# Kernel optimization log

Hardware: AMD Instinct MI355X
Metric: run time of the kernel (lower is better)

## Reference

```python
import jax, jax.numpy as jnp
import numpy as np

COUNT, L1, L2, L3 = 8, 3072, 15, 32


def setup_inputs() -> dict:
    key = jax.random.key(0)
    ks = jax.random.split(key, 10)
    B = 16384
    x = jax.random.uniform(ks[0], (B, L1), dtype=jnp.float32)
    ls_indices = jax.random.randint(ks[1], (B,), 0, COUNT, dtype=jnp.int32)
    s = 1.0 / np.sqrt(L1)
    l1_w = jax.random.uniform(ks[2], (COUNT * (L2 + 1), L1), minval=-s, maxval=s, dtype=jnp.float32)
    l1_b = jax.random.uniform(ks[3], (COUNT * (L2 + 1),), minval=-s, maxval=s, dtype=jnp.float32)
    # l1_fact initialized to zero in the module; use small random values for a
    # meaningful numeric test (same math either way)
    l1f_w = 0.01 * jax.random.normal(ks[4], (L2 + 1, L1), dtype=jnp.float32)
    l1f_b = 0.01 * jax.random.normal(ks[5], (L2 + 1,), dtype=jnp.float32)
    s2 = 1.0 / np.sqrt(2 * L2)
    l2_w = jax.random.uniform(ks[6], (COUNT * L3, 2 * L2), minval=-s2, maxval=s2, dtype=jnp.float32)
    l2_b = jax.random.uniform(ks[7], (COUNT * L3,), minval=-s2, maxval=s2, dtype=jnp.float32)
    s3 = 1.0 / np.sqrt(L3)
    out_w = jax.random.uniform(ks[8], (COUNT, L3), minval=-s3, maxval=s3, dtype=jnp.float32)
    out_b = jnp.zeros((COUNT,), dtype=jnp.float32)
    return {"x": x, "ls_indices": ls_indices, "l1_w": l1_w, "l1_b": l1_b,
            "l1f_w": l1f_w, "l1f_b": l1f_b, "l2_w": l2_w, "l2_b": l2_b,
            "out_w": out_w, "out_b": out_b}


def _gather_bucket(dense, idx):
    # dense: [B, count, F]; idx: [B] -> [B, F]
    return jnp.take_along_axis(dense, idx[:, None, None], axis=1)[:, 0, :]


def reference(x, ls_indices, l1_w, l1_b, l1f_w, l1f_b, l2_w, l2_b, out_w, out_b):
    B = x.shape[0]
    idx = ls_indices.reshape(-1)
    # L1 stage: dense over all buckets, then gather selected bucket
    l1s = (x @ l1_w.T + l1_b).reshape(B, COUNT, L2 + 1)
    l1c = _gather_bucket(l1s, idx)                      # [B, L2+1]
    l1f = x @ l1f_w.T + l1f_b                           # [B, L2+1]
    l1c_main, l1c_out = l1c[:, :L2], l1c[:, L2:]
    l1f_main, l1f_out = l1f[:, :L2], l1f[:, L2:]
    l1x = l1c_main + l1f_main
    # squared-clipped-ReLU pair: [x^2 * 127/128, x] clamped to [0,1]
    l1x = jnp.clip(jnp.concatenate([jnp.square(l1x) * (127.0 / 128.0), l1x], axis=1), 0.0, 1.0)
    # L2 stage
    l2s = (l1x @ l2_w.T + l2_b).reshape(B, COUNT, L3)
    l2x = jnp.clip(_gather_bucket(l2s, idx), 0.0, 1.0)  # [B, L3]
    # output stage
    l3s = (l2x @ out_w.T + out_b).reshape(B, COUNT, 1)
    l3c = _gather_bucket(l3s, idx)                      # [B, 1]
    return l3c + l1f_out + l1c_out
```

## Files before the change

kernel.cpp:

```cpp
#include <hip/hip_runtime.h>
#include <stdint.h>

#define L1D 3072
#define NB 16384
#define CH 16
#define NCHUNK 1032
#define PERM_CAP (NCHUNK * CH)

typedef float  float4v __attribute__((ext_vector_type(4)));
typedef short  short8  __attribute__((ext_vector_type(8)));

__device__ __forceinline__ unsigned short f2bf(float f) {
  uint32_t u = __builtin_bit_cast(uint32_t, f);
  u += 0x7fffu + ((u >> 16) & 1u);
  return (unsigned short)(u >> 16);
}

__global__ void prep_kernel(const float* __restrict__ l1w, const float* __restrict__ l1b,
                            const float* __restrict__ l1fw, const float* __restrict__ l1fb,
                            const int* __restrict__ lsi,
                            unsigned short* __restrict__ cw, float* __restrict__ cb,
                            int* __restrict__ perm, int* __restrict__ desc) {
  if (blockIdx.x < 1536) {
    const int flat = blockIdx.x * 256 + threadIdx.x;
    const int n = flat / L1D;
    const int k = flat - n * L1D;
    cw[flat] = f2bf(l1w[flat] + l1fw[(n & 15) * L1D + k]);
    if (blockIdx.x == 0 && threadIdx.x < 128)
      cb[threadIdx.x] = l1b[threadIdx.x] + l1fb[threadIdx.x & 15];
    return;
  }
  __shared__ int cnt[8], base[8], padded[8], pos[8];
  const int t = threadIdx.x;
  if (t < 8) cnt[t] = 0;
  __syncthreads();
  int loc[8] = {0, 0, 0, 0, 0, 0, 0, 0};
  for (int i = 0; i < NB / 256; ++i) loc[lsi[i * 256 + t]]++;
#pragma unroll
  for (int b = 0; b < 8; ++b) if (loc[b]) atomicAdd(&cnt[b], loc[b]);
  __syncthreads();
  if (t == 0) {
    int off = 0;
    for (int b = 0; b < 8; ++b) {
      base[b] = off;
      padded[b] = (cnt[b] + CH - 1) & ~(CH - 1);
      off += padded[b];
    }
  }
  __syncthreads();
  if (t < 8) pos[t] = base[t];
  for (int i = t; i < PERM_CAP; i += 256) perm[i] = -1;
  for (int g = t; g < NCHUNK; g += 256) {
    int d = -1;
#pragma unroll
    for (int b = 0; b < 8; ++b) {
      const int c0 = base[b] / CH, c1 = (base[b] + padded[b]) / CH;
      if (g >= c0 && g < c1) d = b;
    }
    desc[g] = d;
  }
  __syncthreads();
  for (int i = 0; i < NB / 256; ++i) {
    const int r = i * 256 + t;
    const int p = atomicAdd(&pos[lsi[r]], 1);
    perm[p] = r;
  }
}

__global__ __launch_bounds__(256, 2) void fused_kernel(
    const float* __restrict__ x, const unsigned short* __restrict__ cw,
    const float* __restrict__ cb, const int* __restrict__ perm, const int* __restrict__ desc,
    const float* __restrict__ gl2w, const float* __restrict__ gl2b,
    const float* __restrict__ goutw, const float* __restrict__ goutb,
    float* __restrict__ out) {
  const int b = desc[blockIdx.x];
  if (b < 0) return;
  const int tid = threadIdx.x;
  const int lane = tid & 63;
  const int w = tid >> 6;
  const int col = lane & 15, quad = lane >> 4;

  __shared__ struct {
    float yg[4][CH][17];
    float l2w[32][31];
    float l2b[32], outw[32], bias[16];
    int   prow[CH];
  } sm;

  if (tid < 32) {
    sm.l2b[tid]  = gl2b[b * 32 + tid];
    sm.outw[tid] = goutw[b * 32 + tid];
    if (tid < CH) sm.prow[tid] = perm[blockIdx.x * CH + tid];
    if (tid < 16) sm.bias[tid] = cb[b * 16 + tid];
  }
  for (int i = tid; i < 960; i += 256) {
    const int n = i / 30, k = i - n * 30;
    sm.l2w[n][k] = gl2w[(b * 32 + n) * 30 + k];
  }

  const int ri = perm[blockIdx.x * CH + col];
  const float* ap = x + (size_t)(ri < 0 ? 0 : ri) * L1D + w * 32 + quad * 8;
  const unsigned short* bp = cw + (size_t)(b * 16 + col) * L1D + w * 32 + quad * 8;

  float4v acc = {0.f, 0.f, 0.f, 0.f};
  float4v a0 = *(const float4v*)ap;
  float4v a1 = *(const float4v*)(ap + 4);
  short8  bf = *(const short8*)bp;
#pragma unroll 4
  for (int it = 0; it < 23; ++it) {
    const float* apn = ap + (it + 1) * 128;
    float4v na0 = *(const float4v*)apn;
    float4v na1 = *(const float4v*)(apn + 4);
    short8  nbf = *(const short8*)(bp + (it + 1) * 128);
    short8 af;
    af[0] = (short)f2bf(a0.x); af[1] = (short)f2bf(a0.y);
    af[2] = (short)f2bf(a0.z); af[3] = (short)f2bf(a0.w);
    af[4] = (short)f2bf(a1.x); af[5] = (short)f2bf(a1.y);
    af[6] = (short)f2bf(a1.z); af[7] = (short)f2bf(a1.w);
    acc = __builtin_amdgcn_mfma_f32_16x16x32_bf16(af, bf, acc, 0, 0, 0);
    a0 = na0; a1 = na1; bf = nbf;
  }
  {
    short8 af;
    af[0] = (short)f2bf(a0.x); af[1] = (short)f2bf(a0.y);
    af[2] = (short)f2bf(a0.z); af[3] = (short)f2bf(a0.w);
    af[4] = (short)f2bf(a1.x); af[5] = (short)f2bf(a1.y);
    af[6] = (short)f2bf(a1.z); af[7] = (short)f2bf(a1.w);
    acc = __builtin_amdgcn_mfma_f32_16x16x32_bf16(af, bf, acc, 0, 0, 0);
  }

#pragma unroll
  for (int rg = 0; rg < 4; ++rg) sm.yg[w][quad * 4 + rg][col] = acc[rg];
  __syncthreads();

  {
    const int r = tid >> 4, q = tid & 15;
    const int rr = sm.prow[r];
    float act[30];
#pragma unroll
    for (int c = 0; c < 15; ++c) {
      const float v = sm.yg[0][r][c] + sm.yg[1][r][c] + sm.yg[2][r][c] + sm.yg[3][r][c]
                      + sm.bias[c];
      act[c]      = fminf(v * v * (127.0f / 128.0f), 1.0f);
      act[15 + c] = fminf(fmaxf(v, 0.0f), 1.0f);
    }
    const float y15 = sm.yg[0][r][15] + sm.yg[1][r][15] + sm.yg[2][r][15] + sm.yg[3][r][15]
                      + sm.bias[15];
    float o = 0.0f;
#pragma unroll
    for (int nn = 0; nn < 2; ++nn) {
      const int n = q * 2 + nn;
      float s = sm.l2b[n];
#pragma unroll
      for (int k = 0; k < 30; ++k) s += act[k] * sm.l2w[n][k];
      s = fminf(fmaxf(s, 0.0f), 1.0f);
      o += s * sm.outw[n];
    }
    o += __shfl_down(o, 8, 16);
    o += __shfl_down(o, 4, 16);
    o += __shfl_down(o, 2, 16);
    o += __shfl_down(o, 1, 16);
    if (q == 0 && rr >= 0) out[rr] = o + y15 + goutb[b];
  }
}

extern "C" void kernel_launch(void* const* d_in, const int* in_sizes, int n_in,
                              void* d_out, int out_size, void* d_ws, size_t ws_size,
                              hipStream_t stream) {
  const float* x    = (const float*)d_in[0];
  const int*   lsi  = (const int*)d_in[1];
  const float* l1w  = (const float*)d_in[2];
  const float* l1b  = (const float*)d_in[3];
  const float* l1fw = (const float*)d_in[4];
  const float* l1fb = (const float*)d_in[5];
  const float* l2w  = (const float*)d_in[6];
  const float* l2b  = (const float*)d_in[7];
  const float* outw = (const float*)d_in[8];
  const float* outb = (const float*)d_in[9];
  float* out = (float*)d_out;

  unsigned short* cw = (unsigned short*)d_ws;
  float* cb  = (float*)((char*)d_ws + 786432);
  int*   perm = (int*)((char*)d_ws + 786944);
  int*   desc = (int*)((char*)d_ws + 786944 + PERM_CAP * 4);

  prep_kernel<<<1537, 256, 0, stream>>>(l1w, l1b, l1fw, l1fb, lsi, cw, cb, perm, desc);
  fused_kernel<<<NCHUNK, 256, 0, stream>>>(x, cw, cb, perm, desc, l2w, l2b, outw, outb, out);
}
```

Baseline: 338.8 us.

## Parallelize bucket histogram and row scatter across blocks instead of one serial block

Bucket counting moves into the weight-prep blocks through shared-memory histograms and global atomics. A single-block plan kernel then computes the bucket offsets and the chunk descriptors, and a 64-block scatter kernel writes the permutation with global atomics. Only the padding slots of perm are set to -1, instead of clearing the whole buffer. This removes the long serial single-block pass over all 16384 indices, at the cost of an extra memset and two extra kernel launches.

After: 337.5 us. No clear change (-0.4%).

```diff
diff --git a/kernel.cpp b/kernel.cpp
--- a/kernel.cpp
+++ b/kernel.cpp
@@ -20,51 +20,54 @@
                             const float* __restrict__ l1fw, const float* __restrict__ l1fb,
                             const int* __restrict__ lsi,
                             unsigned short* __restrict__ cw, float* __restrict__ cb,
+                            int* __restrict__ gcnt) {
+  const int flat = blockIdx.x * 256 + threadIdx.x;
+  const int n = flat / L1D;
+  const int k = flat - n * L1D;
+  cw[flat] = f2bf(l1w[flat] + l1fw[(n & 15) * L1D + k]);
+  if (blockIdx.x == 0 && threadIdx.x < 128)
+    cb[threadIdx.x] = l1b[threadIdx.x] + l1fb[threadIdx.x & 15];
+  if (blockIdx.x < 64) {
+    __shared__ int h[8];
+    if (threadIdx.x < 8) h[threadIdx.x] = 0;
+    __syncthreads();
+    atomicAdd(&h[lsi[blockIdx.x * 256 + threadIdx.x]], 1);
+    __syncthreads();
+    if (threadIdx.x < 8) atomicAdd(&gcnt[threadIdx.x * 32], h[threadIdx.x]);
+  }
+}
+
+__global__ void plan_kernel(const int* __restrict__ gcnt, int* __restrict__ gpos,
                             int* __restrict__ perm, int* __restrict__ desc) {
-  if (blockIdx.x < 1536) {
-    const int flat = blockIdx.x * 256 + threadIdx.x;
-    const int n = flat / L1D;
-    const int k = flat - n * L1D;
-    cw[flat] = f2bf(l1w[flat] + l1fw[(n & 15) * L1D + k]);
-    if (blockIdx.x == 0 && threadIdx.x < 128)
-      cb[threadIdx.x] = l1b[threadIdx.x] + l1fb[threadIdx.x & 15];
-    return;
+  const int t = threadIdx.x;
+  int cnt[8], base[8], cb0[8], cb1[8];
+  int off = 0;
+#pragma unroll
+  for (int b = 0; b < 8; ++b) {
+    cnt[b] = gcnt[b * 32];
+    base[b] = off;
+    cb0[b] = off >> 4;
+    off += (cnt[b] + CH - 1) & ~(CH - 1);
+    cb1[b] = off >> 4;
   }
-  __shared__ int cnt[8], base[8], padded[8], pos[8];
-  const int t = threadIdx.x;
-  if (t < 8) cnt[t] = 0;
-  __syncthreads();
-  int loc[8] = {0, 0, 0, 0, 0, 0, 0, 0};
-  for (int i = 0; i < NB / 256; ++i) loc[lsi[i * 256 + t]]++;
-#pragma unroll
-  for (int b = 0; b < 8; ++b) if (loc[b]) atomicAdd(&cnt[b], loc[b]);
-  __syncthreads();
-  if (t == 0) {
-    int off = 0;
-    for (int b = 0; b < 8; ++b) {
-      base[b] = off;
-      padded[b] = (cnt[b] + CH - 1) & ~(CH - 1);
-      off += padded[b];
-    }
+  if (t < 8) {
+    gpos[t * 32] = base[t];
+    const int padded = (cnt[t] + CH - 1) & ~(CH - 1);
+    for (int i = cnt[t]; i < padded; ++i) perm[base[t] + i] = -1;
   }
-  __syncthreads();
-  if (t < 8) pos[t] = base[t];
-  for (int i = t; i < PERM_CAP; i += 256) perm[i] = -1;
   for (int g = t; g < NCHUNK; g += 256) {
     int d = -1;
 #pragma unroll
-    for (int b = 0; b < 8; ++b) {
-      const int c0 = base[b] / CH, c1 = (base[b] + padded[b]) / CH;
-      if (g >= c0 && g < c1) d = b;
-    }
+    for (int b = 0; b < 8; ++b) if (g >= cb0[b] && g < cb1[b]) d = b;
     desc[g] = d;
   }
-  __syncthreads();
-  for (int i = 0; i < NB / 256; ++i) {
-    const int r = i * 256 + t;
-    const int p = atomicAdd(&pos[lsi[r]], 1);
-    perm[p] = r;
-  }
+}
+
+__global__ void scatter_kernel(const int* __restrict__ lsi, int* __restrict__ gpos,
+                               int* __restrict__ perm) {
+  const int r = blockIdx.x * 256 + threadIdx.x;
+  const int p = atomicAdd(&gpos[lsi[r] * 32], 1);
+  perm[p] = r;
 }
 
 __global__ __launch_bounds__(256, 2) void fused_kernel(
@@ -179,11 +182,17 @@
   const float* outb = (const float*)d_in[9];
   float* out = (float*)d_out;
 
-  unsigned short* cw = (unsigned short*)d_ws;
-  float* cb  = (float*)((char*)d_ws + 786432);
-  int*   perm = (int*)((char*)d_ws + 786944);
-  int*   desc = (int*)((char*)d_ws + 786944 + PERM_CAP * 4);
+  char* ws = (char*)d_ws;
+  unsigned short* cw = (unsigned short*)ws;
+  float* cb  = (float*)(ws + 786432);
+  int* gcnt  = (int*)(ws + 786944);
+  int* gpos  = (int*)(ws + 787968);
+  int* perm  = (int*)(ws + 788992);
+  int* desc  = (int*)(ws + 855040);
 
-  prep_kernel<<<1537, 256, 0, stream>>>(l1w, l1b, l1fw, l1fb, lsi, cw, cb, perm, desc);
+  hipMemsetAsync(gcnt, 0, 1024, stream);
+  prep_kernel<<<1536, 256, 0, stream>>>(l1w, l1b, l1fw, l1fb, lsi, cw, cb, gcnt);
+  plan_kernel<<<1, 256, 0, stream>>>(gcnt, gpos, perm, desc);
+  scatter_kernel<<<64, 256, 0, stream>>>(lsi, gpos, perm);
   fused_kernel<<<NCHUNK, 256, 0, stream>>>(x, cw, cb, perm, desc, l2w, l2b, outw, outb, out);
 }
```

## Parallelize bucket sort with global atomics into fixed-capacity per-bucket slots

Applied to the files above, without the earlier changes.

Replaces the single-block counting sort in the prep kernel with 64 blocks that each append row indices into a fixed-capacity slot per bucket, using global atomic counters that a memset clears first. The fused kernel now takes its bucket from the block index and exits early for chunks past that bucket's count, so no descriptor array is needed. This removes the serial one-block tail from the prep stage. In exchange it adds a memset launch, contended global atomics on eight counters, and a larger grid with many idle blocks. It also assumes no bucket holds more than 2560 rows.

Result: no change. 334.3 us (-1.4%).

```diff
diff --git a/kernel.cpp b/kernel.cpp
--- a/kernel.cpp
+++ b/kernel.cpp
@@ -4,8 +4,9 @@
 #define L1D 3072
 #define NB 16384
 #define CH 16
-#define NCHUNK 1032
-#define PERM_CAP (NCHUNK * CH)
+#define CAP 2560
+#define CPB (CAP / CH)
+#define NFUSED (8 * CPB)
 
 typedef float  float4v __attribute__((ext_vector_type(4)));
 typedef short  short8  __attribute__((ext_vector_type(8)));
@@ -20,7 +21,7 @@
                             const float* __restrict__ l1fw, const float* __restrict__ l1fb,
                             const int* __restrict__ lsi,
                             unsigned short* __restrict__ cw, float* __restrict__ cb,
-                            int* __restrict__ perm, int* __restrict__ desc) {
+                            int* __restrict__ cnt, int* __restrict__ perm) {
   if (blockIdx.x < 1536) {
     const int flat = blockIdx.x * 256 + threadIdx.x;
     const int n = flat / L1D;
@@ -28,53 +29,24 @@
     cw[flat] = f2bf(l1w[flat] + l1fw[(n & 15) * L1D + k]);
     if (blockIdx.x == 0 && threadIdx.x < 128)
       cb[threadIdx.x] = l1b[threadIdx.x] + l1fb[threadIdx.x & 15];
-    return;
-  }
-  __shared__ int cnt[8], base[8], padded[8], pos[8];
-  const int t = threadIdx.x;
-  if (t < 8) cnt[t] = 0;
-  __syncthreads();
-  int loc[8] = {0, 0, 0, 0, 0, 0, 0, 0};
-  for (int i = 0; i < NB / 256; ++i) loc[lsi[i * 256 + t]]++;
-#pragma unroll
-  for (int b = 0; b < 8; ++b) if (loc[b]) atomicAdd(&cnt[b], loc[b]);
-  __syncthreads();
-  if (t == 0) {
-    int off = 0;
-    for (int b = 0; b < 8; ++b) {
-      base[b] = off;
-      padded[b] = (cnt[b] + CH - 1) & ~(CH - 1);
-      off += padded[b];
-    }
-  }
-  __syncthreads();
-  if (t < 8) pos[t] = base[t];
-  for (int i = t; i < PERM_CAP; i += 256) perm[i] = -1;
-  for (int g = t; g < NCHUNK; g += 256) {
-    int d = -1;
-#pragma unroll
-    for (int b = 0; b < 8; ++b) {
-      const int c0 = base[b] / CH, c1 = (base[b] + padded[b]) / CH;
-      if (g >= c0 && g < c1) d = b;
-    }
-    desc[g] = d;
-  }
-  __syncthreads();
-  for (int i = 0; i < NB / 256; ++i) {
-    const int r = i * 256 + t;
-    const int p = atomicAdd(&pos[lsi[r]], 1);
-    perm[p] = r;
+  } else {
+    const int r = (blockIdx.x - 1536) * 256 + threadIdx.x;
+    const int b = lsi[r];
+    const int p = atomicAdd(&cnt[b * 32], 1);
+    perm[b * CAP + p] = r;
   }
 }
 
 __global__ __launch_bounds__(256, 2) void fused_kernel(
     const float* __restrict__ x, const unsigned short* __restrict__ cw,
-    const float* __restrict__ cb, const int* __restrict__ perm, const int* __restrict__ desc,
+    const float* __restrict__ cb, const int* __restrict__ perm, const int* __restrict__ cnt,
     const float* __restrict__ gl2w, const float* __restrict__ gl2b,
     const float* __restrict__ goutw, const float* __restrict__ goutb,
     float* __restrict__ out) {
-  const int b = desc[blockIdx.x];
-  if (b < 0) return;
+  const int b = blockIdx.x / CPB;
+  const int local = blockIdx.x - b * CPB;
+  const int cnt_b = cnt[b * 32];
+  if (local * CH >= cnt_b) return;
   const int tid = threadIdx.x;
   const int lane = tid & 63;
   const int w = tid >> 6;
@@ -90,7 +62,8 @@
   if (tid < 32) {
     sm.l2b[tid]  = gl2b[b * 32 + tid];
     sm.outw[tid] = goutw[b * 32 + tid];
-    if (tid < CH) sm.prow[tid] = perm[blockIdx.x * CH + tid];
+    if (tid < CH)
+      sm.prow[tid] = (local * CH + tid < cnt_b) ? perm[b * CAP + local * CH + tid] : -1;
     if (tid < 16) sm.bias[tid] = cb[b * 16 + tid];
   }
   for (int i = tid; i < 960; i += 256) {
@@ -98,7 +71,8 @@
     sm.l2w[n][k] = gl2w[(b * 32 + n) * 30 + k];
   }
 
-  const int ri = perm[blockIdx.x * CH + col];
+  const int idx = local * CH + col;
+  const int ri = (idx < cnt_b) ? perm[b * CAP + idx] : 0;
   const float* ap = x + (size_t)(ri < 0 ? 0 : ri) * L1D + w * 32 + quad * 8;
   const unsigned short* bp = cw + (size_t)(b * 16 + col) * L1D + w * 32 + quad * 8;
 
@@ -179,11 +153,13 @@
   const float* outb = (const float*)d_in[9];
   float* out = (float*)d_out;
 
-  unsigned short* cw = (unsigned short*)d_ws;
-  float* cb  = (float*)((char*)d_ws + 786432);
-  int*   perm = (int*)((char*)d_ws + 786944);
-  int*   desc = (int*)((char*)d_ws + 786944 + PERM_CAP * 4);
+  char* ws = (char*)d_ws;
+  unsigned short* cw = (unsigned short*)ws;
+  float* cb  = (float*)(ws + 786432);
+  int* cnt   = (int*)(ws + 786944);
+  int* perm  = (int*)(ws + 787968);
 
-  prep_kernel<<<1537, 256, 0, stream>>>(l1w, l1b, l1fw, l1fb, lsi, cw, cb, perm, desc);
-  fused_kernel<<<NCHUNK, 256, 0, stream>>>(x, cw, cb, perm, desc, l2w, l2b, outw, outb, out);
+  hipMemsetAsync(cnt, 0, 1024, stream);
+  prep_kernel<<<1600, 256, 0, stream>>>(l1w, l1b, l1fw, l1fb, lsi, cw, cb, cnt, perm);
+  fused_kernel<<<NFUSED, 256, 0, stream>>>(x, cw, cb, perm, cnt, l2w, l2b, outw, outb, out);
 }
```
